# Optimization experiments

Measured on AMD Instinct MI355X. Metric: run time of the kernel, lower is better.

## Reference

```python
import jax, jax.numpy as jnp
import numpy as np

SIGMA = 1.0


def _rbf_kernel(X, sigma):
    # pairwise squared Euclidean distances: ||xi||^2 + ||xj||^2 - 2 xi.xj
    sq = jnp.sum(X * X, axis=1)  # [n]
    d2 = sq[:, None] + sq[None, :] - 2.0 * (X @ X.T)
    d2 = jnp.maximum(d2, 0.0)
    return jnp.exp(-d2 / (2.0 * sigma ** 2))


def _center(K):
    # Kc = H @ K @ H with H = I - 11^T/n, done in O(n^2):
    # Kc = K - row_mean - col_mean + grand_mean
    row_mean = jnp.mean(K, axis=1, keepdims=True)   # [n,1]
    col_mean = jnp.mean(K, axis=0, keepdims=True)   # [1,n]
    grand = jnp.mean(K)
    return K - row_mean - col_mean + grand


def setup_inputs() -> dict:
    key = jax.random.key(0)
    k1, k2 = jax.random.split(key)
    X = jax.random.normal(k1, (8192, 512), dtype=jnp.float32)
    Y = jax.random.normal(k2, (8192, 512), dtype=jnp.float32)
    return {"X": X, "Y": Y}


def reference(X, Y):
    n = X.shape[0]
    K = _rbf_kernel(X, SIGMA)
    L = _rbf_kernel(Y, SIGMA)
    Kc = _center(K)
    Lc = _center(L)
    # trace(Kc @ Lc) == sum(Kc * Lc^T) == sum(Kc * Lc) since Lc symmetric
    hsic_value = jnp.sum(Kc * Lc) / (n - 1) ** 2
    return hsic_value
```

## Files before the change

kernel.cpp:

```cpp
#include <hip/hip_runtime.h>
#include <hip/hip_bf16.h>

#define N 8192
#define D 512

typedef __attribute__((ext_vector_type(4))) float f32x4;
typedef __attribute__((ext_vector_type(2))) long i64x2;

#define WAITVM(n) asm volatile("s_waitcnt vmcnt(" #n ")" ::: "memory")
#define BAR __builtin_amdgcn_s_barrier()

__device__ __forceinline__ void g2l16(const void* g, void* l) {
  __builtin_amdgcn_global_load_lds(
      (const __attribute__((address_space(1))) void*)g,
      (__attribute__((address_space(3))) void*)l, 16, 0, 0);
}

__global__ __launch_bounds__(128) void prep_kernel(
    const float* __restrict__ X, const float* __restrict__ Y,
    unsigned char* __restrict__ Xb, unsigned char* __restrict__ Yb,
    float* __restrict__ sqX, float* __restrict__ sqY) {
  const int b = blockIdx.x;
  const int row = b & (N - 1);
  const float* src = (b < N) ? X : Y;
  unsigned char* dst = (b < N) ? Xb : Yb;
  float* sq = (b < N) ? sqX : sqY;
  const int t = threadIdx.x;
  float4 v = reinterpret_cast<const float4*>(src + (size_t)row * D)[t];
  unsigned p = __builtin_amdgcn_cvt_pk_fp8_f32(v.x, v.y, 0, false);
  p = __builtin_amdgcn_cvt_pk_fp8_f32(v.z, v.w, p, true);
  float f0 = __builtin_amdgcn_cvt_f32_fp8(p, 0);
  float f1 = __builtin_amdgcn_cvt_f32_fp8(p, 1);
  float f2 = __builtin_amdgcn_cvt_f32_fp8(p, 2);
  float f3 = __builtin_amdgcn_cvt_f32_fp8(p, 3);
  float s = f0 * f0 + f1 * f1 + f2 * f2 + f3 * f3;
  const int g = t >> 4;
  const int kl = (t & 15) * 4;
  const int dest = g * 64 + ((kl & 31) >> 3) * 16 + (kl >> 5) * 8 + (kl & 7);
  *reinterpret_cast<unsigned*>(dst + (size_t)row * D + dest) = p;
  #pragma unroll
  for (int msk = 1; msk < 64; msk <<= 1) s += __shfl_xor(s, msk);
  __shared__ float red[2];
  if ((t & 63) == 0) red[t >> 6] = s;
  __syncthreads();
  if (t == 0) sq[row] = red[0] + red[1];
}

__global__ __launch_bounds__(256, 2) void hsic_main(
    const unsigned char* __restrict__ Xb, const unsigned char* __restrict__ Yb,
    const float* __restrict__ sqX, const float* __restrict__ sqY,
    float* __restrict__ rowK, float* __restrict__ rowL,
    float* __restrict__ sums) {
  __shared__ __align__(16) unsigned char sbuf[3][2][128 * 64];

  const int bid = (blockIdx.x & 7) * 260 + (blockIdx.x >> 3);
  int ti = (int)((129.0f - sqrtf(16641.0f - 8.0f * (float)bid)) * 0.5f);
  while (ti > 0 && (ti * (129 - ti)) / 2 > bid) --ti;
  while (((ti + 1) * (128 - ti)) / 2 <= bid) ++ti;
  const int tj = ti + (bid - (ti * (129 - ti)) / 2);
  const bool diag = (ti == tj);

  const int ib = ti * 128, jb = tj * 128;
  const int t = threadIdx.x;
  const int lane = t & 63, wave = t >> 6;
  const int wr = wave >> 1, wc = wave & 1;
  const int fr = lane & 15, fq = lane >> 4;

  f32x4 accK[4][4], accL[4][4];
  #pragma unroll
  for (int m = 0; m < 4; ++m)
    #pragma unroll
    for (int n = 0; n < 4; ++n) { accK[m][n] = (f32x4)0.f; accL[m][n] = (f32x4)0.f; }

  const unsigned char* s0 = Xb + (size_t)ib * D;
  const unsigned char* s1 = Xb + (size_t)jb * D;
  const unsigned char* s2 = Yb + (size_t)ib * D;
  const unsigned char* s3 = Yb + (size_t)jb * D;

  const int srow = t >> 2;
  const int swcb = ((t & 3) * 16) ^ (((t >> 3) & 3) << 4);
  const int lo16 = t * 16;

  auto stage = [&](int ph) {
    const int b = ph % 3;
    const int kt = ph >> 1;
    const unsigned char* si = (ph & 1) ? s2 : s0;
    const unsigned char* sj = (ph & 1) ? s3 : s1;
    #pragma unroll
    for (int q = 0; q < 2; ++q) {
      const size_t goff = (size_t)(q * 64 + srow) * D + kt * 64 + swcb;
      const int lo = q * 4096 + lo16;
      g2l16(si + goff, &sbuf[b][0][lo]);
      g2l16(sj + goff, &sbuf[b][1][lo]);
    }
  };

  const int fcol = (fq * 16) ^ (((fr >> 1) & 3) << 4);

  i64x2 a[4], b[4];
  auto frags = [&](int ph) {
    const unsigned char* si = sbuf[ph % 3][0];
    const unsigned char* sj = sbuf[ph % 3][1];
    #pragma unroll
    for (int m = 0; m < 4; ++m)
      a[m] = *(const i64x2*)&si[(wr * 64 + m * 16 + fr) * 64 + fcol];
    #pragma unroll
    for (int n = 0; n < 4; ++n)
      b[n] = *(const i64x2*)&sj[(wc * 64 + n * 16 + fr) * 64 + fcol];
  };
  auto mmaK = [&]() {
    __builtin_amdgcn_s_setprio(1);
    #pragma unroll
    for (int m = 0; m < 4; ++m)
      #pragma unroll
      for (int n = 0; n < 4; ++n) {
        accK[m][n] = __builtin_amdgcn_mfma_f32_16x16x32_fp8_fp8(a[m][0], b[n][0], accK[m][n], 0, 0, 0);
        accK[m][n] = __builtin_amdgcn_mfma_f32_16x16x32_fp8_fp8(a[m][1], b[n][1], accK[m][n], 0, 0, 0);
      }
    __builtin_amdgcn_s_setprio(0);
  };
  auto mmaL = [&]() {
    __builtin_amdgcn_s_setprio(1);
    #pragma unroll
    for (int m = 0; m < 4; ++m)
      #pragma unroll
      for (int n = 0; n < 4; ++n) {
        accL[m][n] = __builtin_amdgcn_mfma_f32_16x16x32_fp8_fp8(a[m][0], b[n][0], accL[m][n], 0, 0, 0);
        accL[m][n] = __builtin_amdgcn_mfma_f32_16x16x32_fp8_fp8(a[m][1], b[n][1], accL[m][n], 0, 0, 0);
      }
    __builtin_amdgcn_s_setprio(0);
  };

  stage(0); stage(1);
  #pragma unroll 1
  for (int p = 0; p < 14; ++p) {
    WAITVM(4);
    BAR;
    frags(p);
    stage(p + 2);
    if (p & 1) mmaL(); else mmaK();
  }
  WAITVM(4);
  BAR;
  frags(14);
  mmaK();
  WAITVM(0);
  BAR;
  frags(15);
  mmaL();

  float sxj[4], syj[4];
  #pragma unroll
  for (int n = 0; n < 4; ++n) {
    const int j = jb + wc * 64 + n * 16 + fr;
    sxj[n] = sqX[j];
    syj[n] = sqY[j];
  }
  float kl = 0.f;
  float ckK[4] = {0.f, 0.f, 0.f, 0.f}, ckL[4] = {0.f, 0.f, 0.f, 0.f};
  #pragma unroll
  for (int m = 0; m < 4; ++m) {
    #pragma unroll
    for (int r = 0; r < 4; ++r) {
      const int i = ib + wr * 64 + m * 16 + fq * 4 + r;
      const float sxi = sqX[i], syi = sqY[i];
      float rk = 0.f, rl = 0.f;
      #pragma unroll
      for (int n = 0; n < 4; ++n) {
        float dK = fmaxf(sxi + sxj[n] - 2.f * accK[m][n][r], 0.f);
        float Kv = __expf(-0.5f * dK);
        float dL = fmaxf(syi + syj[n] - 2.f * accL[m][n][r], 0.f);
        float Lv = __expf(-0.5f * dL);
        kl += Kv * Lv;
        rk += Kv; rl += Lv;
        ckK[n] += Kv; ckL[n] += Lv;
      }
      #pragma unroll
      for (int msk = 1; msk < 16; msk <<= 1) {
        rk += __shfl_xor(rk, msk);
        rl += __shfl_xor(rl, msk);
      }
      if (fr == 0) {
        atomicAdd(&rowK[i], rk);
        atomicAdd(&rowL[i], rl);
      }
    }
  }
  if (!diag) {
    #pragma unroll
    for (int n = 0; n < 4; ++n) {
      float a2 = ckK[n], b2 = ckL[n];
      a2 += __shfl_xor(a2, 16); a2 += __shfl_xor(a2, 32);
      b2 += __shfl_xor(b2, 16); b2 += __shfl_xor(b2, 32);
      if (fq == 0) {
        const int j = jb + wc * 64 + n * 16 + fr;
        atomicAdd(&rowK[j], a2);
        atomicAdd(&rowL[j], b2);
      }
    }
    kl *= 2.f;
  }
  #pragma unroll
  for (int msk = 1; msk < 64; msk <<= 1) kl += __shfl_xor(kl, msk);
  __shared__ float klred[4];
  if (lane == 0) klred[wave] = kl;
  __syncthreads();
  if (t == 0) atomicAdd(sums, klred[0] + klred[1] + klred[2] + klred[3]);
}

__global__ __launch_bounds__(256) void finalize_kernel(
    const float* __restrict__ rowK, const float* __restrict__ rowL,
    const float* __restrict__ sums, float* __restrict__ out) {
  const int t = threadIdx.x;
  float dp = 0.f, sk = 0.f, sl = 0.f;
  for (int i = t; i < N; i += 256) {
    float a = rowK[i], b = rowL[i];
    dp += a * b; sk += a; sl += b;
  }
  #pragma unroll
  for (int msk = 1; msk < 64; msk <<= 1) {
    dp += __shfl_xor(dp, msk);
    sk += __shfl_xor(sk, msk);
    sl += __shfl_xor(sl, msk);
  }
  __shared__ float r[3][4];
  const int wave = t >> 6, lane = t & 63;
  if (lane == 0) { r[0][wave] = dp; r[1][wave] = sk; r[2][wave] = sl; }
  __syncthreads();
  if (t == 0) {
    float DP = r[0][0] + r[0][1] + r[0][2] + r[0][3];
    float SK = r[1][0] + r[1][1] + r[1][2] + r[1][3];
    float SL = r[2][0] + r[2][1] + r[2][2] + r[2][3];
    const float n = (float)N;
    float raw = sums[0] - (2.f / n) * DP + (SK / n) * (SL / n);
    out[0] = raw / ((n - 1.f) * (n - 1.f));
  }
}

extern "C" void kernel_launch(void* const* d_in, const int* in_sizes, int n_in,
                              void* d_out, int out_size, void* d_ws, size_t ws_size,
                              hipStream_t stream) {
  const float* X = (const float*)d_in[0];
  const float* Y = (const float*)d_in[1];
  char* ws = (char*)d_ws;
  unsigned char* Xb = (unsigned char*)ws;
  unsigned char* Yb = (unsigned char*)(ws + (size_t)N * D);
  float* sqX = (float*)(ws + (size_t)2 * N * D);
  float* sqY = sqX + N;
  float* rowK = sqY + N;
  float* rowL = rowK + N;
  float* sums = rowL + N;

  (void)hipMemsetAsync(rowK, 0, (size_t)(2 * N + 16) * sizeof(float), stream);
  prep_kernel<<<2 * N, 128, 0, stream>>>(X, Y, Xb, Yb, sqX, sqY);
  const int ntiles = (N / 128) * (N / 128 + 1) / 2;
  hsic_main<<<ntiles, 256, 0, stream>>>(Xb, Yb, sqX, sqY, rowK, rowL, sums);
  finalize_kernel<<<1, 256, 0, stream>>>(rowK, rowL, sums, (float*)d_out);
}
```

Before: 164.7 us.

## Use 512-thread blocks with 8 waves and double-buffered combined X/Y staging

Main kernel moves from 256 to 512 threads. Each of the 8 waves now computes a 64x32 sub-tile instead of 64x64, which halves accumulator registers per wave. The staging changes from a 3-deep buffer alternating X and Y phases to a 2-deep buffer that loads all four operand tiles per k-step, with an extra barrier and LDS wait before refilling the buffer. This is meant to raise wave-level parallelism and latency hiding. The cost is more B-fragment LDS reads per MFMA and an added barrier per iteration.

```diff
diff --git a/kernel.cpp b/kernel.cpp
--- a/kernel.cpp
+++ b/kernel.cpp
@@ -8,6 +8,7 @@
 typedef __attribute__((ext_vector_type(2))) long i64x2;
 
 #define WAITVM(n) asm volatile("s_waitcnt vmcnt(" #n ")" ::: "memory")
+#define WAITLGKM asm volatile("s_waitcnt lgkmcnt(0)" ::: "memory")
 #define BAR __builtin_amdgcn_s_barrier()
 
 __device__ __forceinline__ void g2l16(const void* g, void* l) {
@@ -46,12 +47,13 @@
   if (t == 0) sq[row] = red[0] + red[1];
 }
 
-__global__ __launch_bounds__(256, 2) void hsic_main(
+__global__ __launch_bounds__(512) void hsic_main(
     const unsigned char* __restrict__ Xb, const unsigned char* __restrict__ Yb,
     const float* __restrict__ sqX, const float* __restrict__ sqY,
     float* __restrict__ rowK, float* __restrict__ rowL,
     float* __restrict__ sums) {
-  __shared__ __align__(16) unsigned char sbuf[3][2][128 * 64];
+  __shared__ __align__(16) unsigned char sbuf[2][4][128 * 64];
+  __shared__ float klred[8];
 
   const int bid = (blockIdx.x & 7) * 260 + (blockIdx.x >> 3);
   int ti = (int)((129.0f - sqrtf(16641.0f - 8.0f * (float)bid)) * 0.5f);
@@ -63,14 +65,14 @@
   const int ib = ti * 128, jb = tj * 128;
   const int t = threadIdx.x;
   const int lane = t & 63, wave = t >> 6;
-  const int wr = wave >> 1, wc = wave & 1;
+  const int wr = wave >> 2, wc = wave & 3;
   const int fr = lane & 15, fq = lane >> 4;
 
-  f32x4 accK[4][4], accL[4][4];
+  f32x4 accK[4][2], accL[4][2];
   #pragma unroll
   for (int m = 0; m < 4; ++m)
     #pragma unroll
-    for (int n = 0; n < 4; ++n) { accK[m][n] = (f32x4)0.f; accL[m][n] = (f32x4)0.f; }
+    for (int n = 0; n < 2; ++n) { accK[m][n] = (f32x4)0.f; accL[m][n] = (f32x4)0.f; }
 
   const unsigned char* s0 = Xb + (size_t)ib * D;
   const unsigned char* s1 = Xb + (size_t)jb * D;
@@ -79,85 +81,74 @@
 
   const int srow = t >> 2;
   const int swcb = ((t & 3) * 16) ^ (((t >> 3) & 3) << 4);
+  const size_t gbase = (size_t)srow * D + swcb;
   const int lo16 = t * 16;
 
-  auto stage = [&](int ph) {
-    const int b = ph % 3;
-    const int kt = ph >> 1;
-    const unsigned char* si = (ph & 1) ? s2 : s0;
-    const unsigned char* sj = (ph & 1) ? s3 : s1;
-    #pragma unroll
-    for (int q = 0; q < 2; ++q) {
-      const size_t goff = (size_t)(q * 64 + srow) * D + kt * 64 + swcb;
-      const int lo = q * 4096 + lo16;
-      g2l16(si + goff, &sbuf[b][0][lo]);
-      g2l16(sj + goff, &sbuf[b][1][lo]);
-    }
+  auto stage = [&](int kt, int p) {
+    const size_t go = gbase + kt * 64;
+    g2l16(s0 + go, &sbuf[p][0][lo16]);
+    g2l16(s1 + go, &sbuf[p][1][lo16]);
+    g2l16(s2 + go, &sbuf[p][2][lo16]);
+    g2l16(s3 + go, &sbuf[p][3][lo16]);
   };
 
   const int fcol = (fq * 16) ^ (((fr >> 1) & 3) << 4);
 
-  i64x2 a[4], b[4];
-  auto frags = [&](int ph) {
-    const unsigned char* si = sbuf[ph % 3][0];
-    const unsigned char* sj = sbuf[ph % 3][1];
+  i64x2 a[4], b[2];
+  auto frags = [&](int p, int which) {
+    const unsigned char* si = sbuf[p][which * 2];
+    const unsigned char* sj = sbuf[p][which * 2 + 1];
     #pragma unroll
     for (int m = 0; m < 4; ++m)
       a[m] = *(const i64x2*)&si[(wr * 64 + m * 16 + fr) * 64 + fcol];
     #pragma unroll
-    for (int n = 0; n < 4; ++n)
-      b[n] = *(const i64x2*)&sj[(wc * 64 + n * 16 + fr) * 64 + fcol];
+    for (int n = 0; n < 2; ++n)
+      b[n] = *(const i64x2*)&sj[(wc * 32 + n * 16 + fr) * 64 + fcol];
   };
-  auto mmaK = [&]() {
+  auto mmaInto = [&](f32x4 (&acc)[4][2]) {
     __builtin_amdgcn_s_setprio(1);
     #pragma unroll
     for (int m = 0; m < 4; ++m)
       #pragma unroll
-      for (int n = 0; n < 4; ++n) {
-        accK[m][n] = __builtin_amdgcn_mfma_f32_16x16x32_fp8_fp8(a[m][0], b[n][0], accK[m][n], 0, 0, 0);
-        accK[m][n] = __builtin_amdgcn_mfma_f32_16x16x32_fp8_fp8(a[m][1], b[n][1], accK[m][n], 0, 0, 0);
+      for (int n = 0; n < 2; ++n) {
+        acc[m][n] = __builtin_amdgcn_mfma_f32_16x16x32_fp8_fp8(a[m][0], b[n][0], acc[m][n], 0, 0, 0);
+        acc[m][n] = __builtin_amdgcn_mfma_f32_16x16x32_fp8_fp8(a[m][1], b[n][1], acc[m][n], 0, 0, 0);
       }
     __builtin_amdgcn_s_setprio(0);
   };
-  auto mmaL = [&]() {
-    __builtin_amdgcn_s_setprio(1);
-    #pragma unroll
-    for (int m = 0; m < 4; ++m)
-      #pragma unroll
-      for (int n = 0; n < 4; ++n) {
-        accL[m][n] = __builtin_amdgcn_mfma_f32_16x16x32_fp8_fp8(a[m][0], b[n][0], accL[m][n], 0, 0, 0);
-        accL[m][n] = __builtin_amdgcn_mfma_f32_16x16x32_fp8_fp8(a[m][1], b[n][1], accL[m][n], 0, 0, 0);
-      }
-    __builtin_amdgcn_s_setprio(0);
-  };
-
-  stage(0); stage(1);
+
+  stage(0, 0); stage(1, 1);
   #pragma unroll 1
-  for (int p = 0; p < 14; ++p) {
+  for (int kt = 0; kt < 6; ++kt) {
+    const int p = kt & 1;
     WAITVM(4);
     BAR;
-    frags(p);
-    stage(p + 2);
-    if (p & 1) mmaL(); else mmaK();
+    frags(p, 0);
+    mmaInto(accK);
+    frags(p, 1);
+    WAITLGKM;
+    BAR;
+    stage(kt + 2, p);
+    mmaInto(accL);
   }
   WAITVM(4);
   BAR;
-  frags(14);
-  mmaK();
+  frags(0, 0); mmaInto(accK);
+  frags(0, 1); WAITLGKM; mmaInto(accL);
   WAITVM(0);
   BAR;
-  frags(15);
-  mmaL();
-
-  float sxj[4], syj[4];
-  #pragma unroll
-  for (int n = 0; n < 4; ++n) {
-    const int j = jb + wc * 64 + n * 16 + fr;
+  frags(1, 0); mmaInto(accK);
+  frags(1, 1); WAITLGKM; mmaInto(accL);
+
+  float sxj[2], syj[2];
+  #pragma unroll
+  for (int n = 0; n < 2; ++n) {
+    const int j = jb + wc * 32 + n * 16 + fr;
     sxj[n] = sqX[j];
     syj[n] = sqY[j];
   }
   float kl = 0.f;
-  float ckK[4] = {0.f, 0.f, 0.f, 0.f}, ckL[4] = {0.f, 0.f, 0.f, 0.f};
+  float ckK[2] = {0.f, 0.f}, ckL[2] = {0.f, 0.f};
   #pragma unroll
   for (int m = 0; m < 4; ++m) {
     #pragma unroll
@@ -166,7 +157,7 @@
       const float sxi = sqX[i], syi = sqY[i];
       float rk = 0.f, rl = 0.f;
       #pragma unroll
-      for (int n = 0; n < 4; ++n) {
+      for (int n = 0; n < 2; ++n) {
         float dK = fmaxf(sxi + sxj[n] - 2.f * accK[m][n][r], 0.f);
         float Kv = __expf(-0.5f * dK);
         float dL = fmaxf(syi + syj[n] - 2.f * accL[m][n][r], 0.f);
@@ -188,12 +179,12 @@
   }
   if (!diag) {
     #pragma unroll
-    for (int n = 0; n < 4; ++n) {
+    for (int n = 0; n < 2; ++n) {
       float a2 = ckK[n], b2 = ckL[n];
       a2 += __shfl_xor(a2, 16); a2 += __shfl_xor(a2, 32);
       b2 += __shfl_xor(b2, 16); b2 += __shfl_xor(b2, 32);
       if (fq == 0) {
-        const int j = jb + wc * 64 + n * 16 + fr;
+        const int j = jb + wc * 32 + n * 16 + fr;
         atomicAdd(&rowK[j], a2);
         atomicAdd(&rowL[j], b2);
       }
@@ -202,10 +193,14 @@
   }
   #pragma unroll
   for (int msk = 1; msk < 64; msk <<= 1) kl += __shfl_xor(kl, msk);
-  __shared__ float klred[4];
   if (lane == 0) klred[wave] = kl;
   __syncthreads();
-  if (t == 0) atomicAdd(sums, klred[0] + klred[1] + klred[2] + klred[3]);
+  if (t == 0) {
+    float s = 0.f;
+    #pragma unroll
+    for (int w = 0; w < 8; ++w) s += klred[w];
+    atomicAdd(sums, s);
+  }
 }
 
 __global__ __launch_bounds__(256) void finalize_kernel(
@@ -254,6 +249,6 @@
   (void)hipMemsetAsync(rowK, 0, (size_t)(2 * N + 16) * sizeof(float), stream);
   prep_kernel<<<2 * N, 128, 0, stream>>>(X, Y, Xb, Yb, sqX, sqY);
   const int ntiles = (N / 128) * (N / 128 + 1) / 2;
-  hsic_main<<<ntiles, 256, 0, stream>>>(Xb, Yb, sqX, sqY, rowK, rowL, sums);
+  hsic_main<<<ntiles, 512, 0, stream>>>(Xb, Yb, sqX, sqY, rowK, rowL, sums);
   finalize_kernel<<<1, 256, 0, stream>>>(rowK, rowL, sums, (float*)d_out);
 }
```

After: 246.4 us. 49.6% more time.
